# Optimization experiments

Measured on AMD Instinct MI355X. Metric: run time of the kernel, lower is better.

## Reference

```python
import jax, jax.numpy as jnp
import numpy as np

N = 100000   # nodes
R = 4        # relations
E = 200000   # edges per relation
IN = 256
HID = 64
OUT = 64
H = 8        # heads
NEG_SLOPE = 0.2


def setup_inputs() -> dict:
    key = jax.random.key(0)
    ks = jax.random.split(key, 13)
    s = 0.05
    return {
        "x": jax.random.normal(ks[0], (N, IN), jnp.float32),
        "src": jax.random.randint(ks[1], (R, E), 0, N),
        "dst": jax.random.randint(ks[2], (R, E), 0, N),
        "W0": jax.random.normal(ks[3], (R, IN, H * HID), jnp.float32) * s,
        "al0": jax.random.normal(ks[4], (R, H, HID), jnp.float32) * s,
        "ar0": jax.random.normal(ks[5], (R, H, HID), jnp.float32) * s,
        "W1": jax.random.normal(ks[6], (R, H * HID, H * HID), jnp.float32) * s,
        "al1": jax.random.normal(ks[7], (R, H, HID), jnp.float32) * s,
        "ar1": jax.random.normal(ks[8], (R, H, HID), jnp.float32) * s,
        "W2": jax.random.normal(ks[9], (R, H * HID, H * OUT), jnp.float32) * s,
        "al2": jax.random.normal(ks[10], (R, H, OUT), jnp.float32) * s,
        "ar2": jax.random.normal(ks[11], (R, H, OUT), jnp.float32) * s,
    }


def gat_layer(h, src, dst, W, al, ar):
    """Multi-relation GATConv layer; HeteroGraphConv sums ELU'd per-relation outputs.
    h: [N, in]; W: [R, in, H*O]; al/ar: [R, H, O]. Returns [N, H, O]."""
    n = h.shape[0]
    nheads, odim = al.shape[1], al.shape[2]
    acc = jnp.zeros((n, nheads, odim), h.dtype)
    for r in range(W.shape[0]):  # small fixed relation count
        f = (h @ W[r]).reshape(n, nheads, odim)          # [N,H,O]
        el = jnp.sum(f * al[r], axis=-1)                  # [N,H]
        er = jnp.sum(f * ar[r], axis=-1)                  # [N,H]
        s_r, d_r = src[r], dst[r]
        e = jax.nn.leaky_relu(el[s_r] + er[d_r], NEG_SLOPE)  # [E,H]
        # segment softmax over incoming edges per destination node
        m = jax.ops.segment_max(e, d_r, num_segments=n)
        m = jnp.where(jnp.isfinite(m), m, 0.0)
        ex = jnp.exp(e - m[d_r])
        denom = jax.ops.segment_sum(ex, d_r, num_segments=n)
        alpha = ex / (denom[d_r] + 1e-9)                  # [E,H]
        msg = f[s_r] * alpha[:, :, None]                  # [E,H,O]
        out_r = jax.ops.segment_sum(msg, d_r, num_segments=n)  # [N,H,O]
        acc = acc + jax.nn.elu(out_r)
    return acc


def reference(x, src, dst, W0, al0, ar0, W1, al1, ar1, W2, al2, ar2):
    h = gat_layer(x, src, dst, W0, al0, ar0).reshape(N, -1)   # flatten heads
    h = gat_layer(h, src, dst, W1, al1, ar1).reshape(N, -1)   # flatten heads
    h = gat_layer(h, src, dst, W2, al2, ar2).mean(axis=1)     # mean over heads
    return h
```

## Files before the change

### kernel.cpp

```cpp
#include <hip/hip_runtime.h>
#include <hip/hip_bf16.h>
#include <math.h>

#define NNODES 100000
#define NREL 4
#define NEDGE 200000
#define NH 8
#define FDIM 512
#define NMB 782
#define GEMM_GRID (NMB * 4)
#define GEMM_CPX (GEMM_GRID / 8)

typedef float f4 __attribute__((ext_vector_type(4)));
typedef __bf16 bf16x8 __attribute__((ext_vector_type(8)));
typedef __bf16 bf16x4 __attribute__((ext_vector_type(4)));

__device__ __forceinline__ float eluf(float v) { return v > 0.f ? v : expm1f(v); }
__device__ __forceinline__ void gload16(const __bf16* g, __bf16* l) {
  __builtin_amdgcn_global_load_lds((const __attribute__((address_space(1))) void*)g,
                                   (__attribute__((address_space(3))) void*)l, 16, 0, 0);
}

__global__ void k_conv(const float* __restrict__ in, __bf16* __restrict__ outp) {
  int i = (blockIdx.x * 256 + threadIdx.x) * 4;
  f4 v = *(const f4*)(in + i);
  bf16x4 o = {(__bf16)v.x, (__bf16)v.y, (__bf16)v.z, (__bf16)v.w};
  *(bf16x4*)(outp + i) = o;
}
__global__ void k_copyb(const __bf16* __restrict__ in, __bf16* __restrict__ outp) {
  int i = (blockIdx.x * 256 + threadIdx.x) * 8;
  *(bf16x8*)(outp + i) = *(const bf16x8*)(in + i);
}

__global__ void k_transW(const float* __restrict__ W, __bf16* __restrict__ Wt, int K) {
  __shared__ float tile[32][33];
  int r = blockIdx.z;
  const float* Wr = W + (size_t)r * K * FDIM;
  __bf16* Wtr = Wt + (size_t)r * FDIM * K;
  int k0 = blockIdx.x * 32, n0 = blockIdx.y * 32;
  int tx = threadIdx.x, ty = threadIdx.y;
  for (int i = ty; i < 32; i += 8)
    tile[i][tx] = Wr[(size_t)(k0 + i) * FDIM + n0 + tx];
  __syncthreads();
  for (int i = ty; i < 32; i += 8)
    Wtr[(size_t)(n0 + i) * K + k0 + tx] = (__bf16)tile[tx][i];
}

__global__ __launch_bounds__(256) void k_gemm(const __bf16* __restrict__ A,
                                              const __bf16* __restrict__ BT,
                                              __bf16* __restrict__ C,
                                              const float* __restrict__ al,
                                              const float* __restrict__ ar,
                                              float* __restrict__ el,
                                              float* __restrict__ er, int M, int K) {
  __shared__ alignas(16) __bf16 lA[2][128 * 32];
  __shared__ alignas(16) __bf16 lB[2][128 * 32];
  int t = threadIdx.x, l = t & 63, w = t >> 6;
  int bid = blockIdx.x;
  int swz = (bid & 7) * GEMM_CPX + (bid >> 3);
  int m0 = (swz >> 2) * 128, n0 = (swz & 3) * 128;
  int wm = (w >> 1) * 64, wn = (w & 1) * 64;
  f4 acc[4][4] = {};
  int r0 = t >> 2, c0 = t & 3;
  int ra = m0 + r0;      if (ra >= M) ra = M - 1;
  int rb = m0 + r0 + 64; if (rb >= M) rb = M - 1;
  const __bf16* gA0 = A + (size_t)ra * K + c0 * 8;
  const __bf16* gA1 = A + (size_t)rb * K + c0 * 8;
  const __bf16* gB0 = BT + (size_t)(n0 + r0) * K + c0 * 8;
  const __bf16* gB1 = BT + (size_t)(n0 + r0 + 64) * K + c0 * 8;

#define STAGE(buf, k0)                          \
  do {                                          \
    gload16(gA0 + (k0), &lA[buf][t * 8]);       \
    gload16(gA1 + (k0), &lA[buf][(t + 256) * 8]); \
    gload16(gB0 + (k0), &lB[buf][t * 8]);       \
    gload16(gB1 + (k0), &lB[buf][(t + 256) * 8]); \
  } while (0)

  STAGE(0, 0);
  __syncthreads();
  int nt = K >> 5;
  int cur = 0;
  for (int kt = 0; kt < nt; kt++) {
    if (kt + 1 < nt) STAGE(cur ^ 1, (kt + 1) * 32);
    bf16x8 a[4], b[4];
#pragma unroll
    for (int i = 0; i < 4; i++) {
      a[i] = *(const bf16x8*)(&lA[cur][(wm + i * 16 + (l & 15)) * 32 + (l >> 4) * 8]);
      b[i] = *(const bf16x8*)(&lB[cur][(wn + i * 16 + (l & 15)) * 32 + (l >> 4) * 8]);
    }
#pragma unroll
    for (int i = 0; i < 4; i++)
#pragma unroll
      for (int j = 0; j < 4; j++)
        acc[i][j] = __builtin_amdgcn_mfma_f32_16x16x32_bf16(a[i], b[j], acc[i][j], 0, 0, 0);
    __syncthreads();
    cur ^= 1;
  }
#undef STAGE

  int cn = n0 + wn + (l & 15);
  int rbase = m0 + wm + (l >> 4) * 4;
#pragma unroll
  for (int i = 0; i < 4; i++)
#pragma unroll
    for (int j = 0; j < 4; j++)
#pragma unroll
      for (int q = 0; q < 4; q++) {
        int row = rbase + i * 16 + q;
        if (row < M) C[(size_t)row * FDIM + cn + j * 16] = (__bf16)acc[i][j][q];
      }

  int h = (n0 + wn) >> 6;
  float av[4], bv[4];
#pragma unroll
  for (int j = 0; j < 4; j++) {
    av[j] = al[h * 64 + j * 16 + (l & 15)];
    bv[j] = ar[h * 64 + j * 16 + (l & 15)];
  }
#pragma unroll
  for (int i = 0; i < 4; i++)
#pragma unroll
    for (int q = 0; q < 4; q++) {
      float se = acc[i][0][q] * av[0] + acc[i][1][q] * av[1] +
                 acc[i][2][q] * av[2] + acc[i][3][q] * av[3];
      float sr = acc[i][0][q] * bv[0] + acc[i][1][q] * bv[1] +
                 acc[i][2][q] * bv[2] + acc[i][3][q] * bv[3];
      se += __shfl_xor(se, 1); se += __shfl_xor(se, 2);
      se += __shfl_xor(se, 4); se += __shfl_xor(se, 8);
      sr += __shfl_xor(sr, 1); sr += __shfl_xor(sr, 2);
      sr += __shfl_xor(sr, 4); sr += __shfl_xor(sr, 8);
      if ((l & 15) == 0) {
        int row = rbase + i * 16 + q;
        if (row < M) { el[row * 8 + h] = se; er[row * 8 + h] = sr; }
      }
    }
}

__global__ void k_count(const int* __restrict__ dst, int* __restrict__ deg) {
  int e = blockIdx.x * 256 + threadIdx.x;
  int r = blockIdx.y;
  if (e < NEDGE) {
    int d = dst[(size_t)r * NEDGE + e];
    if ((unsigned)d < (unsigned)NNODES) atomicAdd(&deg[r * NNODES + d], 1);
  }
}

__global__ __launch_bounds__(256) void k_scan_a(const int* __restrict__ in, int* __restrict__ out,
                                                int* __restrict__ bsum, int n) {
  __shared__ int wsums[4];
  int t = threadIdx.x, lane = t & 63, w = t >> 6;
  int base = blockIdx.x * 1024 + t * 4;
  int v0 = base + 0 < n ? in[base + 0] : 0;
  int v1 = base + 1 < n ? in[base + 1] : 0;
  int v2 = base + 2 < n ? in[base + 2] : 0;
  int v3 = base + 3 < n ? in[base + 3] : 0;
  int tot = v0 + v1 + v2 + v3;
  int sc = tot;
#pragma unroll
  for (int off = 1; off < 64; off <<= 1) {
    int u = __shfl_up(sc, off);
    if (lane >= off) sc += u;
  }
  if (lane == 63) wsums[w] = sc;
  __syncthreads();
  int add = 0;
#pragma unroll
  for (int i = 0; i < 4; i++)
    if (i < w) add += wsums[i];
  int excl = add + sc - tot;
  if (base + 0 < n) out[base + 0] = excl;
  if (base + 1 < n) out[base + 1] = excl + v0;
  if (base + 2 < n) out[base + 2] = excl + v0 + v1;
  if (base + 3 < n) out[base + 3] = excl + v0 + v1 + v2;
  if (t == 255) bsum[blockIdx.x] = add + sc;
}

__global__ __launch_bounds__(256) void k_scan_b(int* __restrict__ bsum, int nb) {
  __shared__ int wsums[4];
  int t = threadIdx.x, lane = t & 63, w = t >> 6;
  int i0 = t * 2, i1 = t * 2 + 1;
  int v0 = i0 < nb ? bsum[i0] : 0;
  int v1 = i1 < nb ? bsum[i1] : 0;
  int tot = v0 + v1, sc = tot;
#pragma unroll
  for (int off = 1; off < 64; off <<= 1) {
    int u = __shfl_up(sc, off);
    if (lane >= off) sc += u;
  }
  if (lane == 63) wsums[w] = sc;
  __syncthreads();
  int add = 0;
#pragma unroll
  for (int i = 0; i < 4; i++)
    if (i < w) add += wsums[i];
  int excl = add + sc - tot;
  if (i0 < nb) bsum[i0] = excl;
  if (i1 < nb) bsum[i1] = excl + v0;
}

__global__ void k_scan_c(int* __restrict__ out, const int* __restrict__ bsum, int n) {
  int i = blockIdx.x * 256 + threadIdx.x;
  if (i < n) out[i] += bsum[i >> 10];
}

__global__ void k_scatter(const int* __restrict__ src, const int* __restrict__ dst,
                          const int* __restrict__ ptrf, int* __restrict__ cur,
                          int* __restrict__ csrc) {
  int e = blockIdx.x * 256 + threadIdx.x;
  int r = blockIdx.y;
  if (e >= NEDGE) return;
  int d = dst[(size_t)r * NEDGE + e];
  if ((unsigned)d >= (unsigned)NNODES) return;
  int slot = ptrf[r * NNODES + d] + atomicAdd(&cur[r * NNODES + d], 1);
  if ((unsigned)slot < (unsigned)(NREL * NEDGE))
    csrc[slot] = src[(size_t)r * NEDGE + e];
}

__global__ void k_agg(const __bf16* __restrict__ f, const float* __restrict__ el,
                      const float* __restrict__ er, const int* __restrict__ ptrf,
                      const int* __restrict__ deg, const int* __restrict__ csrc,
                      __bf16* __restrict__ accG) {
  int t = threadIdx.x;
  int l = t & 63;
  int d = blockIdx.x * 4 + (t >> 6);
  int cnt = deg[d];
  if (cnt <= 0) return;
  int start = ptrf[d];
  if (start < 0) start = 0;
  if (start > NREL * NEDGE) start = NREL * NEDGE;
  if (cnt > NREL * NEDGE - start) cnt = NREL * NEDGE - start;
  int h = l >> 3;
  float erh = er[d * 8 + h];
  float a[8] = {0.f, 0.f, 0.f, 0.f, 0.f, 0.f, 0.f, 0.f};
  float den = 0.f;
  for (int j = 0; j < cnt; j++) {
    int s = csrc[start + j];
    if ((unsigned)s >= (unsigned)NNODES) s = 0;
    float e = el[s * 8 + h] + erh;
    e = (e > 0.f) ? e : 0.2f * e;
    float ex = __expf(e);
    den += ex;
    bf16x8 fv = *(const bf16x8*)(f + (size_t)s * FDIM + l * 8);
#pragma unroll
    for (int i = 0; i < 8; i++) a[i] += ex * (float)fv[i];
  }
  float inv = 1.f / (den + 1e-9f);
  __bf16* ap = accG + (size_t)d * FDIM + l * 8;
  bf16x8 cv = *(bf16x8*)ap;
  bf16x8 o;
#pragma unroll
  for (int i = 0; i < 8; i++) o[i] = (__bf16)((float)cv[i] + eluf(a[i] * inv));
  *(bf16x8*)ap = o;
}

__global__ void k_mean(const __bf16* __restrict__ acc, float* __restrict__ out) {
  int t = blockIdx.x * 256 + threadIdx.x;
  int n = t >> 6, o = t & 63;
  const __bf16* ap = acc + (size_t)n * FDIM + o;
  float s = 0.f;
#pragma unroll
  for (int h = 0; h < 8; h++) s += (float)ap[h * 64];
  out[t] = s * 0.125f;
}

extern "C" void kernel_launch(void* const* d_in, const int* in_sizes, int n_in,
                              void* d_out, int out_size, void* d_ws, size_t ws_size,
                              hipStream_t stream) {
  const float* x = (const float*)d_in[0];
  const int* srcp = (const int*)d_in[1];
  const int* dstp = (const int*)d_in[2];
  const float* Wl[3]  = {(const float*)d_in[3], (const float*)d_in[6], (const float*)d_in[9]};
  const float* alp[3] = {(const float*)d_in[4], (const float*)d_in[7], (const float*)d_in[10]};
  const float* arl[3] = {(const float*)d_in[5], (const float*)d_in[8], (const float*)d_in[11]};
  float* out = (float*)d_out;
  (void)in_sizes; (void)n_in; (void)out_size;

  auto rup = [](size_t b) { return (b + 255) & ~(size_t)255; };
  size_t need = rup((size_t)NNODES * FDIM * 2) * 3 +
                rup((size_t)NNODES * NH * 4) * 2 +
                rup((size_t)NREL * FDIM * FDIM * 2) +
                rup((size_t)NREL * NNODES * 4) * 3 +
                rup((size_t)NREL * NEDGE * 4) + rup(4096);
  if (ws_size < need) return;

  char* ws = (char*)d_ws;
  size_t off = 0;
  auto alloc = [&](size_t bytes) -> void* { void* p = ws + off; off += rup(bytes); return p; };
  __bf16* hb   = (__bf16*)alloc((size_t)NNODES * FDIM * 2);
  __bf16* fbuf = (__bf16*)alloc((size_t)NNODES * FDIM * 2);
  __bf16* accG = (__bf16*)alloc((size_t)NNODES * FDIM * 2);
  float* el    = (float*)alloc((size_t)NNODES * NH * 4);
  float* er    = (float*)alloc((size_t)NNODES * NH * 4);
  __bf16* Wt   = (__bf16*)alloc((size_t)NREL * FDIM * FDIM * 2);
  int* deg  = (int*)alloc((size_t)NREL * NNODES * 4);
  int* ptrf = (int*)alloc((size_t)NREL * NNODES * 4);
  int* cur  = (int*)alloc((size_t)NREL * NNODES * 4);
  int* csrc = (int*)alloc((size_t)NREL * NEDGE * 4);
  int* bsum = (int*)alloc(4096);

  hipMemsetAsync(deg, 0, (size_t)NREL * NNODES * 4, stream);
  hipMemsetAsync(cur, 0, (size_t)NREL * NNODES * 4, stream);
  k_count<<<dim3((NEDGE + 255) / 256, NREL), 256, 0, stream>>>(dstp, deg);
  int ntot = NREL * NNODES;
  int nb1 = (ntot + 1023) / 1024;
  k_scan_a<<<nb1, 256, 0, stream>>>(deg, ptrf, bsum, ntot);
  k_scan_b<<<1, 256, 0, stream>>>(bsum, nb1);
  k_scan_c<<<(ntot + 255) / 256, 256, 0, stream>>>(ptrf, bsum, ntot);
  k_scatter<<<dim3((NEDGE + 255) / 256, NREL), 256, 0, stream>>>(srcp, dstp, ptrf, cur, csrc);

  for (int L = 0; L < 3; L++) {
    int K = (L == 0) ? 256 : FDIM;
    if (L == 0)
      k_conv<<<(NNODES * 256) / 1024, 256, 0, stream>>>(x, hb);
    else
      k_copyb<<<(NNODES * 512) / 2048, 256, 0, stream>>>(accG, hb);
    k_transW<<<dim3(K / 32, 16, NREL), dim3(32, 8), 0, stream>>>(Wl[L], Wt, K);
    hipMemsetAsync(accG, 0, (size_t)NNODES * FDIM * 2, stream);
    for (int r = 0; r < NREL; r++) {
      k_gemm<<<GEMM_GRID, 256, 0, stream>>>(hb, Wt + (size_t)r * FDIM * K, fbuf,
                                            alp[L] + r * 512, arl[L] + r * 512,
                                            el, er, NNODES, K);
      k_agg<<<NNODES / 4, 256, 0, stream>>>(fbuf, el, er, ptrf + r * NNODES,
                                            deg + r * NNODES, csrc, accG);
    }
  }
  k_mean<<<(NNODES * 64) / 256, 256, 0, stream>>>(accG, out);
}
```

Before: 2.251 ms.

## Batch all relations into one wide GEMM and triple-buffer the GEMM k-loop

When the workspace is large enough, one GEMM launch now computes all four relation projections into a single [N, 2048] feature buffer, and the aggregation kernels read their slice through stride and offset parameters. This reads the activation matrix once instead of four times and cuts the GEMM launch count. The GEMM main loop moves from double to triple buffering, with explicit vmcnt waits and barriers, so global-to-LDS loads run further ahead of the MFMAs. In exchange the feature buffer is four times larger and more costly to keep in cache, and the kernel falls back to per-relation launches when the workspace is too small.

```diff
diff --git a/kernel.cpp b/kernel.cpp
--- a/kernel.cpp
+++ b/kernel.cpp
@@ -8,8 +8,6 @@
 #define NH 8
 #define FDIM 512
 #define NMB 782
-#define GEMM_GRID (NMB * 4)
-#define GEMM_CPX (GEMM_GRID / 8)
 
 typedef float f4 __attribute__((ext_vector_type(4)));
 typedef __bf16 bf16x8 __attribute__((ext_vector_type(8)));
@@ -52,13 +50,17 @@
                                               const float* __restrict__ al,
                                               const float* __restrict__ ar,
                                               float* __restrict__ el,
-                                              float* __restrict__ er, int M, int K) {
-  __shared__ alignas(16) __bf16 lA[2][128 * 32];
-  __shared__ alignas(16) __bf16 lB[2][128 * 32];
+                                              float* __restrict__ er, int M, int K,
+                                              int nb4shift, int cpx) {
+  __shared__ alignas(16) __bf16 lA[3][128 * 32];
+  __shared__ alignas(16) __bf16 lB[3][128 * 32];
   int t = threadIdx.x, l = t & 63, w = t >> 6;
   int bid = blockIdx.x;
-  int swz = (bid & 7) * GEMM_CPX + (bid >> 3);
-  int m0 = (swz >> 2) * 128, n0 = (swz & 3) * 128;
+  int swz = (bid & 7) * cpx + (bid >> 3);
+  int nb4mask = (1 << nb4shift) - 1;
+  int m0 = (swz >> nb4shift) * 128, n0 = (swz & nb4mask) * 128;
+  int NDIM = 128 << nb4shift;
+  int nh_tot = 2 << nb4shift;
   int wm = (w >> 1) * 64, wn = (w & 1) * 64;
   f4 acc[4][4] = {};
   int r0 = t >> 2, c0 = t & 3;
@@ -69,33 +71,40 @@
   const __bf16* gB0 = BT + (size_t)(n0 + r0) * K + c0 * 8;
   const __bf16* gB1 = BT + (size_t)(n0 + r0 + 64) * K + c0 * 8;
 
-#define STAGE(buf, k0)                          \
-  do {                                          \
-    gload16(gA0 + (k0), &lA[buf][t * 8]);       \
-    gload16(gA1 + (k0), &lA[buf][(t + 256) * 8]); \
-    gload16(gB0 + (k0), &lB[buf][t * 8]);       \
-    gload16(gB1 + (k0), &lB[buf][(t + 256) * 8]); \
+#define STAGE(buf, kk)                              \
+  do {                                              \
+    gload16(gA0 + (kk), &lA[buf][t * 8]);           \
+    gload16(gA1 + (kk), &lA[buf][(t + 256) * 8]);   \
+    gload16(gB0 + (kk), &lB[buf][t * 8]);           \
+    gload16(gB1 + (kk), &lB[buf][(t + 256) * 8]);   \
   } while (0)
 
+  int nt = K >> 5;
   STAGE(0, 0);
-  __syncthreads();
-  int nt = K >> 5;
+  STAGE(1, 32);
+  STAGE(2, 64);
   int cur = 0;
   for (int kt = 0; kt < nt; kt++) {
-    if (kt + 1 < nt) STAGE(cur ^ 1, (kt + 1) * 32);
+    int rem = nt - 1 - kt;
+    if (rem >= 2)      asm volatile("s_waitcnt vmcnt(8)" ::: "memory");
+    else if (rem == 1) asm volatile("s_waitcnt vmcnt(4)" ::: "memory");
+    else               asm volatile("s_waitcnt vmcnt(0)" ::: "memory");
+    __builtin_amdgcn_s_barrier();
     bf16x8 a[4], b[4];
 #pragma unroll
     for (int i = 0; i < 4; i++) {
       a[i] = *(const bf16x8*)(&lA[cur][(wm + i * 16 + (l & 15)) * 32 + (l >> 4) * 8]);
       b[i] = *(const bf16x8*)(&lB[cur][(wn + i * 16 + (l & 15)) * 32 + (l >> 4) * 8]);
     }
+    asm volatile("s_waitcnt lgkmcnt(0)" ::: "memory");
+    __builtin_amdgcn_s_barrier();
+    if (kt + 3 < nt) STAGE(cur, (kt + 3) * 32);
 #pragma unroll
     for (int i = 0; i < 4; i++)
 #pragma unroll
       for (int j = 0; j < 4; j++)
         acc[i][j] = __builtin_amdgcn_mfma_f32_16x16x32_bf16(a[i], b[j], acc[i][j], 0, 0, 0);
-    __syncthreads();
-    cur ^= 1;
+    cur = (cur == 2) ? 0 : cur + 1;
   }
 #undef STAGE
 
@@ -108,7 +117,7 @@
 #pragma unroll
       for (int q = 0; q < 4; q++) {
         int row = rbase + i * 16 + q;
-        if (row < M) C[(size_t)row * FDIM + cn + j * 16] = (__bf16)acc[i][j][q];
+        if (row < M) C[(size_t)row * NDIM + cn + j * 16] = (__bf16)acc[i][j][q];
       }
 
   int h = (n0 + wn) >> 6;
@@ -132,7 +141,7 @@
       sr += __shfl_xor(sr, 4); sr += __shfl_xor(sr, 8);
       if ((l & 15) == 0) {
         int row = rbase + i * 16 + q;
-        if (row < M) { el[row * 8 + h] = se; er[row * 8 + h] = sr; }
+        if (row < M) { el[row * nh_tot + h] = se; er[row * nh_tot + h] = sr; }
       }
     }
 }
@@ -220,7 +229,7 @@
 __global__ void k_agg(const __bf16* __restrict__ f, const float* __restrict__ el,
                       const float* __restrict__ er, const int* __restrict__ ptrf,
                       const int* __restrict__ deg, const int* __restrict__ csrc,
-                      __bf16* __restrict__ accG) {
+                      __bf16* __restrict__ accG, int fstride, int coff, int estride, int eoff) {
   int t = threadIdx.x;
   int l = t & 63;
   int d = blockIdx.x * 4 + (t >> 6);
@@ -231,17 +240,17 @@
   if (start > NREL * NEDGE) start = NREL * NEDGE;
   if (cnt > NREL * NEDGE - start) cnt = NREL * NEDGE - start;
   int h = l >> 3;
-  float erh = er[d * 8 + h];
+  float erh = er[d * estride + eoff + h];
   float a[8] = {0.f, 0.f, 0.f, 0.f, 0.f, 0.f, 0.f, 0.f};
   float den = 0.f;
   for (int j = 0; j < cnt; j++) {
     int s = csrc[start + j];
     if ((unsigned)s >= (unsigned)NNODES) s = 0;
-    float e = el[s * 8 + h] + erh;
+    float e = el[s * estride + eoff + h] + erh;
     e = (e > 0.f) ? e : 0.2f * e;
     float ex = __expf(e);
     den += ex;
-    bf16x8 fv = *(const bf16x8*)(f + (size_t)s * FDIM + l * 8);
+    bf16x8 fv = *(const bf16x8*)(f + (size_t)s * fstride + coff + l * 8);
 #pragma unroll
     for (int i = 0; i < 8; i++) a[i] += ex * (float)fv[i];
   }
@@ -277,21 +286,32 @@
   (void)in_sizes; (void)n_in; (void)out_size;
 
   auto rup = [](size_t b) { return (b + 255) & ~(size_t)255; };
-  size_t need = rup((size_t)NNODES * FDIM * 2) * 3 +
-                rup((size_t)NNODES * NH * 4) * 2 +
-                rup((size_t)NREL * FDIM * FDIM * 2) +
-                rup((size_t)NREL * NNODES * 4) * 3 +
-                rup((size_t)NREL * NEDGE * 4) + rup(4096);
-  if (ws_size < need) return;
+  size_t sz_hin  = rup((size_t)NNODES * FDIM * 2);
+  size_t sz_acc  = rup((size_t)NNODES * FDIM * 2);
+  size_t sz_Wt   = rup((size_t)NREL * FDIM * FDIM * 2);
+  size_t sz_int  = rup((size_t)NREL * NNODES * 4);
+  size_t sz_csrc = rup((size_t)NREL * NEDGE * 4);
+  size_t base_need = sz_hin + sz_acc + sz_Wt + 3 * sz_int + sz_csrc + rup(4096);
+  size_t need_big   = base_need + rup((size_t)NNODES * 2048 * 2) + 2 * rup((size_t)NNODES * 32 * 4);
+  size_t need_small = base_need + rup((size_t)NNODES * 512 * 2)  + 2 * rup((size_t)NNODES * 8 * 4);
+  bool big;
+  if (ws_size >= need_big) big = true;
+  else if (ws_size >= need_small) big = false;
+  else return;
+
+  int nb = big ? 4 : 1;
+  int nb4shift = big ? 4 : 2;
+  int ncols = nb * FDIM;
+  int nheads = nb * NH;
 
   char* ws = (char*)d_ws;
   size_t off = 0;
   auto alloc = [&](size_t bytes) -> void* { void* p = ws + off; off += rup(bytes); return p; };
-  __bf16* hb   = (__bf16*)alloc((size_t)NNODES * FDIM * 2);
-  __bf16* fbuf = (__bf16*)alloc((size_t)NNODES * FDIM * 2);
+  __bf16* hin  = (__bf16*)alloc((size_t)NNODES * FDIM * 2);
   __bf16* accG = (__bf16*)alloc((size_t)NNODES * FDIM * 2);
-  float* el    = (float*)alloc((size_t)NNODES * NH * 4);
-  float* er    = (float*)alloc((size_t)NNODES * NH * 4);
+  __bf16* fbuf = (__bf16*)alloc((size_t)NNODES * ncols * 2);
+  float* el    = (float*)alloc((size_t)NNODES * nheads * 4);
+  float* er    = (float*)alloc((size_t)NNODES * nheads * 4);
   __bf16* Wt   = (__bf16*)alloc((size_t)NREL * FDIM * FDIM * 2);
   int* deg  = (int*)alloc((size_t)NREL * NNODES * 4);
   int* ptrf = (int*)alloc((size_t)NREL * NNODES * 4);
@@ -311,18 +331,22 @@
 
   for (int L = 0; L < 3; L++) {
     int K = (L == 0) ? 256 : FDIM;
-    if (L == 0)
-      k_conv<<<(NNODES * 256) / 1024, 256, 0, stream>>>(x, hb);
-    else
-      k_copyb<<<(NNODES * 512) / 2048, 256, 0, stream>>>(accG, hb);
+    if (L == 0) k_conv<<<(NNODES * 256) / 1024, 256, 0, stream>>>(x, hin);
+    else        k_copyb<<<(NNODES * 512) / 2048, 256, 0, stream>>>(accG, hin);
     k_transW<<<dim3(K / 32, 16, NREL), dim3(32, 8), 0, stream>>>(Wl[L], Wt, K);
     hipMemsetAsync(accG, 0, (size_t)NNODES * FDIM * 2, stream);
-    for (int r = 0; r < NREL; r++) {
-      k_gemm<<<GEMM_GRID, 256, 0, stream>>>(hb, Wt + (size_t)r * FDIM * K, fbuf,
-                                            alp[L] + r * 512, arl[L] + r * 512,
-                                            el, er, NNODES, K);
-      k_agg<<<NNODES / 4, 256, 0, stream>>>(fbuf, el, er, ptrf + r * NNODES,
-                                            deg + r * NNODES, csrc, accG);
+    int ngrid = NMB * 4 * nb;
+    int cpx = ngrid / 8;
+    for (int g = 0; g < NREL / nb; g++) {
+      k_gemm<<<ngrid, 256, 0, stream>>>(hin, Wt + (size_t)g * nb * FDIM * K, fbuf,
+                                        alp[L] + g * nb * 512, arl[L] + g * nb * 512,
+                                        el, er, NNODES, K, nb4shift, cpx);
+      for (int q = 0; q < nb; q++) {
+        int r = g * nb + q;
+        k_agg<<<NNODES / 4, 256, 0, stream>>>(fbuf, el, er, ptrf + r * NNODES,
+                                              deg + r * NNODES, csrc, accG,
+                                              ncols, q * FDIM, nheads, q * NH);
+      }
     }
   }
   k_mean<<<(NNODES * 64) / 256, 256, 0, stream>>>(accG, out);
```

After: 2.222 ms. No clear change (-1.3%).
